# Kernel optimization log

Hardware: AMD Instinct MI355X
Metric: run time of the kernel (lower is better)

## Reference

```python
import jax, jax.numpy as jnp
import numpy as np

B, T, OB, AC, OBL, ACL, W = 2048, 128, 64, 8, 32, 16, 64
DT = 0.05   # spacing of save times
K = 2       # fixed Dopri5 substeps per interval (step size = ode_dt0 = 0.025)


def _mlp2(x, W0, b0, W1, b1):
    # eqx.nn.MLP with depth=1: in -> width (relu) -> out (identity)
    return jax.nn.relu(x @ W0.T + b0) @ W1.T + b1


def setup_inputs() -> dict:
    key = jax.random.key(0)
    ks = jax.random.split(key, 10)
    def lin(k, o, i, scale=1.0):
        return (jax.random.normal(k, (o, i), jnp.float32) * (scale / np.sqrt(i))).astype(jnp.float32)
    return {
        "encW0": lin(ks[0], W, OB), "encb0": jnp.zeros((W,), jnp.float32),
        "encW1": lin(ks[1], OBL, W), "encb1": jnp.zeros((OBL,), jnp.float32),
        "acW0": lin(ks[2], W, AC), "acb0": jnp.zeros((W,), jnp.float32),
        "acW1": lin(ks[3], ACL, W), "acb1": jnp.zeros((ACL,), jnp.float32),
        "dynW0": lin(ks[4], W, OBL + ACL), "dynb0": jnp.zeros((W,), jnp.float32),
        "dynW1": lin(ks[5], OBL, W, 0.5), "dynb1": jnp.zeros((OBL,), jnp.float32),
        "decW0": lin(ks[6], W, OBL), "decb0": jnp.zeros((W,), jnp.float32),
        "decW1": lin(ks[7], OB, W), "decb1": jnp.zeros((OB,), jnp.float32),
        "ob": jax.random.normal(ks[8], (B, OB), jnp.float32),
        "acs": jax.random.normal(ks[9], (B, T, AC), jnp.float32),
        "times": jnp.tile(jnp.arange(T, dtype=jnp.float32) * DT, (B, 1)),
    }


def _dopri5_step(f, t, y, h):
    k1 = f(t, y)
    k2 = f(t + h * (1. / 5.), y + h * ((1. / 5.) * k1))
    k3 = f(t + h * (3. / 10.), y + h * ((3. / 40.) * k1 + (9. / 40.) * k2))
    k4 = f(t + h * (4. / 5.), y + h * ((44. / 45.) * k1 - (56. / 15.) * k2 + (32. / 9.) * k3))
    k5 = f(t + h * (8. / 9.), y + h * ((19372. / 6561.) * k1 - (25360. / 2187.) * k2
                                       + (64448. / 6561.) * k3 - (212. / 729.) * k4))
    k6 = f(t + h, y + h * ((9017. / 3168.) * k1 - (355. / 33.) * k2 + (46732. / 5247.) * k3
                           + (49. / 176.) * k4 - (5103. / 18656.) * k5))
    return y + h * ((35. / 384.) * k1 + (500. / 1113.) * k3 + (125. / 192.) * k4
                    - (2187. / 6784.) * k5 + (11. / 84.) * k6)


def reference(encW0, encb0, encW1, encb1, acW0, acb0, acW1, acb1,
              dynW0, dynb0, dynW1, dynb1, decW0, decb0, decW1, decb1,
              ob, acs, times):
    ac_latents = _mlp2(acs, acW0, acb0, acW1, acb1)   # (B, T, ACL)
    y0 = _mlp2(ob, encW0, encb0, encW1, encb1)        # (B, OBL)

    def single(y0_i, acl_i, t_i):
        n = t_i.shape[0]

        def f(t, y):
            # piecewise-constant action latent: index of save-interval containing t
            idx = jnp.clip(jnp.searchsorted(t_i, t, side='right') - 1, 0, n - 1)
            return _mlp2(jnp.concatenate([y, acl_i[idx]]), dynW0, dynb0, dynW1, dynb1)

        def interval(y, tt):
            t0, t1 = tt
            h = (t1 - t0) / K
            def sub(yc, j):
                return _dopri5_step(f, t0 + j * h, yc, h), None
            y, _ = jax.lax.scan(sub, y, jnp.arange(K, dtype=t_i.dtype))
            return y, y

        _, ys = jax.lax.scan(interval, y0_i, (t_i[:-1], t_i[1:]))
        return jnp.concatenate([y0_i[None], ys], axis=0)   # (T, OBL)

    ys = jax.vmap(single)(y0, ac_latents, times)            # (B, T, OBL)
    return _mlp2(ys, decW0, decb0, decW1, decb1)            # (B, T, OB)
```

## Files before the change

kernel.cpp:

```cpp
#include <hip/hip_runtime.h>

#define NB 2048
#define NT 128

typedef float v2f __attribute__((ext_vector_type(2)));

static __device__ __forceinline__ v2f pkfma(v2f a, v2f b, v2f c) {
#if __has_builtin(__builtin_elementwise_fma)
    return __builtin_elementwise_fma(a, b, c);
#else
    v2f r; r.x = fmaf(a.x, b.x, c.x); r.y = fmaf(a.y, b.y, c.y); return r;
#endif
}
static __device__ __forceinline__ v2f mkv2(float x, float y) { v2f r; r.x = x; r.y = y; return r; }

__global__ __launch_bounds__(256, 4) void acl_kernel(
    const float* __restrict__ acs, const float* __restrict__ acW0,
    const float* __restrict__ acb0, const float* __restrict__ acW1,
    const float* __restrict__ acb1, float* __restrict__ aclout)
{
    __shared__ float sW0[64 * 8];
    __shared__ float sW1[16 * 64];
    __shared__ float sB0[64];
    __shared__ float sB1[16];
    const int tid = threadIdx.x;
    for (int i = tid; i < 64 * 8; i += 256) sW0[i] = acW0[i];
    for (int i = tid; i < 16 * 64; i += 256) sW1[i] = acW1[i];
    if (tid < 64) sB0[tid] = acb0[tid];
    if (tid < 16) sB1[tid] = acb1[tid];
    __syncthreads();

    const int row = blockIdx.x * 256 + tid;
    const float4 x0 = *(const float4*)&acs[row * 8];
    const float4 x1 = *(const float4*)&acs[row * 8 + 4];

    float o[16];
    #pragma unroll
    for (int m = 0; m < 16; ++m) o[m] = sB1[m];

    #pragma unroll
    for (int jc = 0; jc < 16; ++jc) {
        float hq[4];
        #pragma unroll
        for (int u = 0; u < 4; ++u) {
            const int j = jc * 4 + u;
            const float4 wa = *(const float4*)&sW0[j * 8];
            const float4 wb = *(const float4*)&sW0[j * 8 + 4];
            float hv = sB0[j];
            hv = fmaf(x0.x, wa.x, hv); hv = fmaf(x0.y, wa.y, hv);
            hv = fmaf(x0.z, wa.z, hv); hv = fmaf(x0.w, wa.w, hv);
            hv = fmaf(x1.x, wb.x, hv); hv = fmaf(x1.y, wb.y, hv);
            hv = fmaf(x1.z, wb.z, hv); hv = fmaf(x1.w, wb.w, hv);
            hq[u] = fmaxf(hv, 0.f);
        }
        #pragma unroll
        for (int m = 0; m < 16; ++m) {
            const float4 wv = *(const float4*)&sW1[m * 64 + jc * 4];
            o[m] = fmaf(hq[0], wv.x, o[m]);
            o[m] = fmaf(hq[1], wv.y, o[m]);
            o[m] = fmaf(hq[2], wv.z, o[m]);
            o[m] = fmaf(hq[3], wv.w, o[m]);
        }
    }
    float4* op = (float4*)&aclout[row * 16];
    op[0] = make_float4(o[0],  o[1],  o[2],  o[3]);
    op[1] = make_float4(o[4],  o[5],  o[6],  o[7]);
    op[2] = make_float4(o[8],  o[9],  o[10], o[11]);
    op[3] = make_float4(o[12], o[13], o[14], o[15]);
}

__global__ __launch_bounds__(256, 2) void ode_kernel(
    const float* __restrict__ encW0, const float* __restrict__ encb0,
    const float* __restrict__ encW1, const float* __restrict__ encb1,
    const float* __restrict__ dynW0, const float* __restrict__ dynb0,
    const float* __restrict__ dynW1, const float* __restrict__ dynb1,
    const float* __restrict__ ob,    const float* __restrict__ times,
    const float* __restrict__ aclws, float* __restrict__ yio)
{
    __shared__ float sEncW0T[64 * 64];
    __shared__ float sEncW1T[64 * 32];
    __shared__ float sW0s[64 * 32];
    __shared__ float sW1T[64 * 32];
    __shared__ float sM[64 * 64];
    __shared__ float sEncB0[64], sEncB1[32], sB1d[32];
    __shared__ float xbuf[4][64];
    __shared__ float hbuf[4][64];
    __shared__ float tbuf[4][NT];

    const int tid = threadIdx.x;
    for (int i = tid; i < 64 * 64; i += 256) { int r = i >> 6, c = i & 63; sEncW0T[c * 64 + r] = encW0[i]; }
    for (int i = tid; i < 32 * 64; i += 256) { int r = i >> 6, c = i & 63; sEncW1T[c * 32 + r] = encW1[i]; }
    for (int i = tid; i < 64 * 32; i += 256) { int j = i >> 5, mm = i & 31; sW0s[i] = dynW0[j * 48 + mm]; }
    for (int i = tid; i < 64 * 32; i += 256) { int c = i >> 5, mm = i & 31; sW1T[i] = dynW1[mm * 64 + c]; }
    if (tid < 64) { sEncB0[tid] = encb0[tid]; }
    if (tid < 32) { sEncB1[tid] = encb1[tid]; sB1d[tid] = dynb1[tid]; }
    __syncthreads();

    {
        const int j  = tid >> 2;
        const int cg = (tid & 3) * 16;
        float4 wr[8];
        #pragma unroll
        for (int q = 0; q < 8; ++q) wr[q] = *(const float4*)&sW0s[j * 32 + q * 4];
        #pragma unroll 2
        for (int k = 0; k < 16; ++k) {
            const int c = cg + k;
            v2f s0 = mkv2(0.f, 0.f), s1 = mkv2(0.f, 0.f);
            #pragma unroll
            for (int q = 0; q < 8; ++q) {
                const float4 t4 = *(const float4*)&sW1T[c * 32 + q * 4];
                s0 = pkfma(mkv2(t4.x, t4.y), mkv2(wr[q].x, wr[q].y), s0);
                s1 = pkfma(mkv2(t4.z, t4.w), mkv2(wr[q].z, wr[q].w), s1);
            }
            sM[j * 64 + c] = (s0.x + s1.x) + (s0.y + s1.y);
        }
    }
    __syncthreads();

    const int w    = tid >> 6;
    const int lane = tid & 63;
    const int bu   = __builtin_amdgcn_readfirstlane(blockIdx.x * 4 + w);
    const int m    = lane & 31;
    const int H    = lane & 32;

    float* __restrict__ xb = xbuf[w];
    float* __restrict__ hb = hbuf[w];

    float Mf[64];
    #pragma unroll
    for (int q = 0; q < 16; ++q) *(float4*)&Mf[q * 4] = *(const float4*)&sM[lane * 64 + q * 4];
    const v2f* Mp = (const v2f*)Mf;

    float w1rf[32];
    #pragma unroll
    for (int q = 0; q < 8; ++q)  *(float4*)&w1rf[q * 4] = *(const float4*)&dynW1[m * 64 + H + q * 4];
    const v2f* w1r = (const v2f*)w1rf;

    float wa[16];
    #pragma unroll
    for (int q = 0; q < 4; ++q) *(float4*)&wa[q * 4] = *(const float4*)&dynW0[lane * 48 + 32 + q * 4];
    const float b0r = dynb0[lane];
    const float b1r = dynb1[m];

    float vj = 0.f;
    #pragma unroll
    for (int q = 0; q < 8; ++q) {
        const float4 wv = *(const float4*)&dynW0[lane * 48 + q * 4];
        vj = fmaf(wv.x, sB1d[q * 4 + 0], vj); vj = fmaf(wv.y, sB1d[q * 4 + 1], vj);
        vj = fmaf(wv.z, sB1d[q * 4 + 2], vj); vj = fmaf(wv.w, sB1d[q * 4 + 3], vj);
    }

    tbuf[w][lane]      = times[bu * NT + lane];
    tbuf[w][64 + lane] = times[bu * NT + 64 + lane];
    __builtin_amdgcn_wave_barrier();

    auto gproj = [&](float hsv) -> float {
        __builtin_amdgcn_wave_barrier();
        hb[lane] = hsv;
        __builtin_amdgcn_wave_barrier();
        v2f A0 = mkv2(0.f, 0.f), A1 = mkv2(0.f, 0.f);
        v2f A2 = mkv2(0.f, 0.f), A3 = mkv2(0.f, 0.f);
        #pragma unroll
        for (int c = 0; c < 2; ++c) {
            float hr[32];
            #pragma unroll
            for (int q = 0; q < 8; ++q) *(float4*)&hr[q * 4] = *(const float4*)&hb[c * 32 + q * 4];
            const v2f* hp = (const v2f*)hr;
            const v2f* mp = Mp + c * 16;
            #pragma unroll
            for (int q = 0; q < 16; q += 4) {
                A0 = pkfma(hp[q],     mp[q],     A0);
                A1 = pkfma(hp[q + 1], mp[q + 1], A1);
                A2 = pkfma(hp[q + 2], mp[q + 2], A2);
                A3 = pkfma(hp[q + 3], mp[q + 3], A3);
            }
        }
        const v2f S = (A0 + A1) + (A2 + A3);
        return S.x + S.y + vj;
    };

    float y;
    {
        xb[lane] = ob[bu * 64 + lane];
        __builtin_amdgcn_wave_barrier();
        float4 xv[16];
        #pragma unroll
        for (int q = 0; q < 16; ++q) xv[q] = *(const float4*)&xb[q * 4];
        float a0 = sEncB0[lane], a1 = 0.f, a2 = 0.f, a3 = 0.f;
        #pragma unroll
        for (int q = 0; q < 16; ++q) {
            a0 = fmaf(xv[q].x, sEncW0T[(q * 4 + 0) * 64 + lane], a0);
            a1 = fmaf(xv[q].y, sEncW0T[(q * 4 + 1) * 64 + lane], a1);
            a2 = fmaf(xv[q].z, sEncW0T[(q * 4 + 2) * 64 + lane], a2);
            a3 = fmaf(xv[q].w, sEncW0T[(q * 4 + 3) * 64 + lane], a3);
        }
        const float hj = fmaxf((a0 + a1) + (a2 + a3), 0.f);
        hb[lane] = hj;
        __builtin_amdgcn_wave_barrier();
        float4 hv[8];
        #pragma unroll
        for (int q = 0; q < 8; ++q) hv[q] = *(const float4*)&hb[H + q * 4];
        float c0 = 0.f, c1 = 0.f, c2 = 0.f, c3 = 0.f;
        #pragma unroll
        for (int q = 0; q < 8; ++q) {
            c0 = fmaf(hv[q].x, sEncW1T[(H + q * 4 + 0) * 32 + m], c0);
            c1 = fmaf(hv[q].y, sEncW1T[(H + q * 4 + 1) * 32 + m], c1);
            c2 = fmaf(hv[q].z, sEncW1T[(H + q * 4 + 2) * 32 + m], c2);
            c3 = fmaf(hv[q].w, sEncW1T[(H + q * 4 + 3) * 32 + m], c3);
        }
        float part = (c0 + c1) + (c2 + c3);
        part += __shfl_xor(part, 32, 64);
        y = part + sEncB1[m];
    }

    float ystar = 0.f;
    {
        __builtin_amdgcn_wave_barrier();
        xb[m] = y;
        __builtin_amdgcn_wave_barrier();
        #pragma unroll
        for (int q = 0; q < 8; ++q) {
            const float4 wv = *(const float4*)&dynW0[lane * 48 + q * 4];
            const float4 xv = *(const float4*)&xb[q * 4];
            ystar = fmaf(wv.x, xv.x, ystar); ystar = fmaf(wv.y, xv.y, ystar);
            ystar = fmaf(wv.z, xv.z, ystar); ystar = fmaf(wv.w, xv.w, ystar);
        }
    }

    auto acl_part = [&](const float* __restrict__ ap) -> float {
        float ar[16];
        #pragma unroll
        for (int q = 0; q < 4; ++q) *(float4*)&ar[q * 4] = *(const float4*)&ap[q * 4];
        const v2f* a2 = (const v2f*)ar;
        const v2f* wq = (const v2f*)wa;
        v2f s0 = mkv2(0.f, 0.f), s1 = mkv2(0.f, 0.f);
        #pragma unroll
        for (int q = 0; q < 8; q += 2) {
            s0 = pkfma(a2[q],     wq[q],     s0);
            s1 = pkfma(a2[q + 1], wq[q + 1], s1);
        }
        const v2f s = s0 + s1;
        return s.x + s.y;
    };

    auto store_y = [&](float yv, int t) {
        if (lane < 32) yio[(size_t)(bu * NT + t) * 64 + lane] = yv;
    };

    float aclPartC = acl_part(aclws + (size_t)(bu * NT) * 16);
    store_y(y, 0);

    for (int i = 0; i < NT - 1; ++i) {
        const float t0v = tbuf[w][i];
        const float t1v = tbuf[w][i + 1];
        const float hh  = (t1v - t0v) * 0.5f;
        const float aclPartN = acl_part(aclws + (size_t)(bu * NT + i + 1) * 16);
        float haccS = 0.f;

        #pragma unroll 1
        for (int sub = 0; sub < 2; ++sub) {
            const float tsub  = t0v + (float)sub * hh;
            const bool  swap6 = (tsub + hh >= t1v);

            const float a1v = ystar + b0r + aclPartC;

            const float h1 = fmaxf(a1v, 0.f);
            const float g1 = hh * gproj(h1);
            const float h2 = fmaxf(fmaf(0.2f, g1, a1v), 0.f);
            const float g2 = hh * gproj(h2);
            const float h3 = fmaxf(fmaf(0.075f, g1, fmaf(0.225f, g2, a1v)), 0.f);
            const float g3 = hh * gproj(h3);
            const float h4 = fmaxf(
                fmaf((float)(44.0/45.0), g1,
                fmaf((float)(-56.0/15.0), g2,
                fmaf((float)(32.0/9.0), g3, a1v))), 0.f);
            const float g4 = hh * gproj(h4);
            const float h5 = fmaxf(
                fmaf((float)(19372.0/6561.0), g1,
                fmaf((float)(-25360.0/2187.0), g2,
                fmaf((float)(64448.0/6561.0), g3,
                fmaf((float)(-212.0/729.0), g4, a1v)))), 0.f);
            const float g5 = hh * gproj(h5);
            float a6v =
                fmaf((float)(9017.0/3168.0), g1,
                fmaf((float)(-355.0/33.0), g2,
                fmaf((float)(46732.0/5247.0), g3,
                fmaf((float)(49.0/176.0), g4,
                fmaf((float)(-5103.0/18656.0), g5, a1v)))));
            a6v += swap6 ? (aclPartN - aclPartC) : 0.f;
            const float h6 = fmaxf(a6v, 0.f);

            float ha = (float)(35.0/384.0) * h1;
            ha = fmaf((float)(500.0/1113.0),   h3, ha);
            ha = fmaf((float)(125.0/192.0),    h4, ha);
            ha = fmaf((float)(-2187.0/6784.0), h5, ha);
            ha = fmaf((float)(11.0/84.0),      h6, ha);

            const float gacc = gproj(ha);
            ystar = fmaf(hh, gacc, ystar);
            haccS += ha;
        }

        {
            __builtin_amdgcn_wave_barrier();
            hb[lane] = haccS;
            __builtin_amdgcn_wave_barrier();
            float hr[32];
            #pragma unroll
            for (int q = 0; q < 8; ++q) *(float4*)&hr[q * 4] = *(const float4*)&hb[H + q * 4];
            const v2f* hp = (const v2f*)hr;
            v2f c0 = mkv2(0.f, 0.f), c1 = mkv2(0.f, 0.f);
            #pragma unroll
            for (int q = 0; q < 16; q += 2) {
                c0 = pkfma(hp[q],     w1r[q],     c0);
                c1 = pkfma(hp[q + 1], w1r[q + 1], c1);
            }
            float part = (c0.x + c1.x) + (c0.y + c1.y);
            part += __shfl_xor(part, 32, 64);
            y = fmaf(hh, part + 2.f * b1r, y);
        }
        aclPartC = aclPartN;
        store_y(y, i + 1);
    }
}

__global__ __launch_bounds__(256, 2) void dec_kernel(
    const float* __restrict__ decW0, const float* __restrict__ decb0,
    const float* __restrict__ decW1, const float* __restrict__ decb1,
    float* __restrict__ yio)
{
    __shared__ float sW0[64 * 32];
    __shared__ float sW1T[64 * 64];
    __shared__ float sB0[64];
    __shared__ float sB1[64];
    const int tid = threadIdx.x;
    for (int i = tid; i < 64 * 32; i += 256) sW0[i] = decW0[i];
    for (int i = tid; i < 64 * 64; i += 256) { int n = i >> 6, j = i & 63; sW1T[j * 64 + n] = decW1[i]; }
    if (tid < 64) { sB0[tid] = decb0[tid]; sB1[tid] = decb1[tid]; }
    __syncthreads();

    const size_t row = (size_t)blockIdx.x * 256 + tid;
    float* rp = &yio[row * 64];

    float xr[32];
    #pragma unroll
    for (int q = 0; q < 8; ++q) *(float4*)&xr[q * 4] = *(const float4*)&rp[q * 4];

    v2f o2[32];
    #pragma unroll
    for (int n = 0; n < 32; ++n) o2[n] = mkv2(sB1[2 * n], sB1[2 * n + 1]);

    #pragma unroll 4
    for (int j = 0; j < 64; ++j) {
        v2f a0 = mkv2(sB0[j], 0.f), a1 = mkv2(0.f, 0.f);
        #pragma unroll
        for (int q = 0; q < 8; ++q) {
            const float4 wv = *(const float4*)&sW0[j * 32 + q * 4];
            a0 = pkfma(*(const v2f*)&xr[q * 4],     mkv2(wv.x, wv.y), a0);
            a1 = pkfma(*(const v2f*)&xr[q * 4 + 2], mkv2(wv.z, wv.w), a1);
        }
        const float hj = fmaxf((a0.x + a1.x) + (a0.y + a1.y), 0.f);
        const v2f h2 = mkv2(hj, hj);
        #pragma unroll
        for (int q = 0; q < 16; ++q) {
            const float4 wv = *(const float4*)&sW1T[j * 64 + q * 4];
            o2[2 * q]     = pkfma(h2, mkv2(wv.x, wv.y), o2[2 * q]);
            o2[2 * q + 1] = pkfma(h2, mkv2(wv.z, wv.w), o2[2 * q + 1]);
        }
    }

    #pragma unroll
    for (int q = 0; q < 16; ++q)
        *(float4*)&rp[q * 4] = make_float4(o2[2 * q].x, o2[2 * q].y,
                                           o2[2 * q + 1].x, o2[2 * q + 1].y);
}

extern "C" void kernel_launch(void* const* d_in, const int* in_sizes, int n_in,
                              void* d_out, int out_size, void* d_ws, size_t ws_size,
                              hipStream_t stream)
{
    const float* encW0 = (const float*)d_in[0];
    const float* encb0 = (const float*)d_in[1];
    const float* encW1 = (const float*)d_in[2];
    const float* encb1 = (const float*)d_in[3];
    const float* acW0  = (const float*)d_in[4];
    const float* acb0  = (const float*)d_in[5];
    const float* acW1  = (const float*)d_in[6];
    const float* acb1  = (const float*)d_in[7];
    const float* dynW0 = (const float*)d_in[8];
    const float* dynb0 = (const float*)d_in[9];
    const float* dynW1 = (const float*)d_in[10];
    const float* dynb1 = (const float*)d_in[11];
    const float* decW0 = (const float*)d_in[12];
    const float* decb0 = (const float*)d_in[13];
    const float* decW1 = (const float*)d_in[14];
    const float* decb1 = (const float*)d_in[15];
    const float* ob    = (const float*)d_in[16];
    const float* acs   = (const float*)d_in[17];
    const float* times = (const float*)d_in[18];
    float* out = (float*)d_out;
    float* acl = (float*)d_ws;

    acl_kernel<<<(NB * NT) / 256, 256, 0, stream>>>(acs, acW0, acb0, acW1, acb1, acl);
    ode_kernel<<<NB / 4, 256, 0, stream>>>(encW0, encb0, encW1, encb1,
                                           dynW0, dynb0, dynW1, dynb1,
                                           ob, times, acl, out);
    dec_kernel<<<(NB * NT) / 256, 256, 0, stream>>>(decW0, decb0, decW1, decb1, out);
}
```

Measured before the change: 689.5 us.

## Process two batch elements per wavefront in ODE kernel to reuse register weights

Each wavefront now integrates two independent trajectories together, interleaving their RK stages so every projection matvec reuses the register-resident M and W1 weights for both. The intent is to amortise weight register loads and expose independent instruction-level parallelism that hides the LDS and sequential-dependency latency of the stage chain. Grid is halved to NB/8 blocks and launch bounds drop to one block per CU minimum, which raises register pressure and reduces the number of wavefronts available for latency hiding. With 256 blocks on a 256-CU part, each CU gets only a single block.

```diff
diff --git a/kernel.cpp b/kernel.cpp
--- a/kernel.cpp
+++ b/kernel.cpp
@@ -69,7 +69,7 @@
     op[3] = make_float4(o[12], o[13], o[14], o[15]);
 }
 
-__global__ __launch_bounds__(256, 2) void ode_kernel(
+__global__ __launch_bounds__(256, 1) void ode_kernel(
     const float* __restrict__ encW0, const float* __restrict__ encb0,
     const float* __restrict__ encW1, const float* __restrict__ encb1,
     const float* __restrict__ dynW0, const float* __restrict__ dynb0,
@@ -83,15 +83,16 @@
     __shared__ float sW1T[64 * 32];
     __shared__ float sM[64 * 64];
     __shared__ float sEncB0[64], sEncB1[32], sB1d[32];
-    __shared__ float xbuf[4][64];
-    __shared__ float hbuf[4][64];
-    __shared__ float tbuf[4][NT];
+    __shared__ float xbuf[8][64];
+    __shared__ float hbuf[8][64];
+    __shared__ float tbuf[8 * NT];
 
     const int tid = threadIdx.x;
     for (int i = tid; i < 64 * 64; i += 256) { int r = i >> 6, c = i & 63; sEncW0T[c * 64 + r] = encW0[i]; }
     for (int i = tid; i < 32 * 64; i += 256) { int r = i >> 6, c = i & 63; sEncW1T[c * 32 + r] = encW1[i]; }
     for (int i = tid; i < 64 * 32; i += 256) { int j = i >> 5, mm = i & 31; sW0s[i] = dynW0[j * 48 + mm]; }
     for (int i = tid; i < 64 * 32; i += 256) { int c = i >> 5, mm = i & 31; sW1T[i] = dynW1[mm * 64 + c]; }
+    for (int i = tid; i < 8 * NT; i += 256) tbuf[i] = times[(size_t)blockIdx.x * 8 * NT + i];
     if (tid < 64) { sEncB0[tid] = encb0[tid]; }
     if (tid < 32) { sEncB1[tid] = encb1[tid]; sB1d[tid] = dynb1[tid]; }
     __syncthreads();
@@ -119,12 +120,16 @@
 
     const int w    = tid >> 6;
     const int lane = tid & 63;
-    const int bu   = __builtin_amdgcn_readfirstlane(blockIdx.x * 4 + w);
+    const int e0   = w * 2;
+    const int bu0  = __builtin_amdgcn_readfirstlane(blockIdx.x * 8 + e0);
+    const int bu1  = bu0 + 1;
     const int m    = lane & 31;
     const int H    = lane & 32;
 
-    float* __restrict__ xb = xbuf[w];
-    float* __restrict__ hb = hbuf[w];
+    float* __restrict__ xbA = xbuf[e0];
+    float* __restrict__ xbB = xbuf[e0 + 1];
+    float* __restrict__ hbA = hbuf[e0];
+    float* __restrict__ hbB = hbuf[e0 + 1];
 
     float Mf[64];
     #pragma unroll
@@ -150,37 +155,39 @@
         vj = fmaf(wv.z, sB1d[q * 4 + 2], vj); vj = fmaf(wv.w, sB1d[q * 4 + 3], vj);
     }
 
-    tbuf[w][lane]      = times[bu * NT + lane];
-    tbuf[w][64 + lane] = times[bu * NT + 64 + lane];
-    __builtin_amdgcn_wave_barrier();
-
-    auto gproj = [&](float hsv) -> float {
-        __builtin_amdgcn_wave_barrier();
-        hb[lane] = hsv;
+    auto gproj2 = [&](float hA, float hB, float& gA, float& gB) {
+        __builtin_amdgcn_wave_barrier();
+        hbA[lane] = hA;
+        hbB[lane] = hB;
         __builtin_amdgcn_wave_barrier();
         v2f A0 = mkv2(0.f, 0.f), A1 = mkv2(0.f, 0.f);
-        v2f A2 = mkv2(0.f, 0.f), A3 = mkv2(0.f, 0.f);
-        #pragma unroll
-        for (int c = 0; c < 2; ++c) {
-            float hr[32];
-            #pragma unroll
-            for (int q = 0; q < 8; ++q) *(float4*)&hr[q * 4] = *(const float4*)&hb[c * 32 + q * 4];
-            const v2f* hp = (const v2f*)hr;
-            const v2f* mp = Mp + c * 16;
-            #pragma unroll
-            for (int q = 0; q < 16; q += 4) {
-                A0 = pkfma(hp[q],     mp[q],     A0);
-                A1 = pkfma(hp[q + 1], mp[q + 1], A1);
-                A2 = pkfma(hp[q + 2], mp[q + 2], A2);
-                A3 = pkfma(hp[q + 3], mp[q + 3], A3);
+        v2f B0 = mkv2(0.f, 0.f), B1 = mkv2(0.f, 0.f);
+        #pragma unroll
+        for (int c = 0; c < 4; ++c) {
+            float hrA[16], hrB[16];
+            #pragma unroll
+            for (int q = 0; q < 4; ++q) *(float4*)&hrA[q * 4] = *(const float4*)&hbA[c * 16 + q * 4];
+            #pragma unroll
+            for (int q = 0; q < 4; ++q) *(float4*)&hrB[q * 4] = *(const float4*)&hbB[c * 16 + q * 4];
+            const v2f* hpA = (const v2f*)hrA;
+            const v2f* hpB = (const v2f*)hrB;
+            const v2f* mp  = Mp + c * 8;
+            #pragma unroll
+            for (int q = 0; q < 8; q += 2) {
+                A0 = pkfma(hpA[q],     mp[q],     A0);
+                A1 = pkfma(hpA[q + 1], mp[q + 1], A1);
+                B0 = pkfma(hpB[q],     mp[q],     B0);
+                B1 = pkfma(hpB[q + 1], mp[q + 1], B1);
             }
         }
-        const v2f S = (A0 + A1) + (A2 + A3);
-        return S.x + S.y + vj;
+        const v2f SA = A0 + A1;
+        const v2f SB = B0 + B1;
+        gA = SA.x + SA.y + vj;
+        gB = SB.x + SB.y + vj;
     };
 
-    float y;
-    {
+    auto encode = [&](int bu, float* xb, float* hb) -> float {
+        __builtin_amdgcn_wave_barrier();
         xb[lane] = ob[bu * 64 + lane];
         __builtin_amdgcn_wave_barrier();
         float4 xv[16];
@@ -195,6 +202,7 @@
             a3 = fmaf(xv[q].w, sEncW0T[(q * 4 + 3) * 64 + lane], a3);
         }
         const float hj = fmaxf((a0 + a1) + (a2 + a3), 0.f);
+        __builtin_amdgcn_wave_barrier();
         hb[lane] = hj;
         __builtin_amdgcn_wave_barrier();
         float4 hv[8];
@@ -210,22 +218,28 @@
         }
         float part = (c0 + c1) + (c2 + c3);
         part += __shfl_xor(part, 32, 64);
-        y = part + sEncB1[m];
-    }
-
-    float ystar = 0.f;
-    {
-        __builtin_amdgcn_wave_barrier();
-        xb[m] = y;
-        __builtin_amdgcn_wave_barrier();
+        return part + sEncB1[m];
+    };
+
+    auto ystar_init = [&](float yv, float* xb) -> float {
+        __builtin_amdgcn_wave_barrier();
+        xb[m] = yv;
+        __builtin_amdgcn_wave_barrier();
+        float ys = 0.f;
         #pragma unroll
         for (int q = 0; q < 8; ++q) {
             const float4 wv = *(const float4*)&dynW0[lane * 48 + q * 4];
             const float4 xv = *(const float4*)&xb[q * 4];
-            ystar = fmaf(wv.x, xv.x, ystar); ystar = fmaf(wv.y, xv.y, ystar);
-            ystar = fmaf(wv.z, xv.z, ystar); ystar = fmaf(wv.w, xv.w, ystar);
-        }
-    }
+            ys = fmaf(wv.x, xv.x, ys); ys = fmaf(wv.y, xv.y, ys);
+            ys = fmaf(wv.z, xv.z, ys); ys = fmaf(wv.w, xv.w, ys);
+        }
+        return ys;
+    };
+
+    float yA = encode(bu0, xbA, hbA);
+    float yB = encode(bu1, xbB, hbB);
+    float ystarA = ystar_init(yA, xbA);
+    float ystarB = ystar_init(yB, xbB);
 
     auto acl_part = [&](const float* __restrict__ ap) -> float {
         float ar[16];
@@ -243,84 +257,141 @@
         return s.x + s.y;
     };
 
-    auto store_y = [&](float yv, int t) {
+    auto store_y = [&](float yv, int bu, int t) {
         if (lane < 32) yio[(size_t)(bu * NT + t) * 64 + lane] = yv;
     };
 
-    float aclPartC = acl_part(aclws + (size_t)(bu * NT) * 16);
-    store_y(y, 0);
+    float aclCA = acl_part(aclws + (size_t)(bu0 * NT) * 16);
+    float aclCB = acl_part(aclws + (size_t)(bu1 * NT) * 16);
+    store_y(yA, bu0, 0);
+    store_y(yB, bu1, 0);
+
+    const int tb0 = e0 * NT;
+    const int tb1 = (e0 + 1) * NT;
 
     for (int i = 0; i < NT - 1; ++i) {
-        const float t0v = tbuf[w][i];
-        const float t1v = tbuf[w][i + 1];
-        const float hh  = (t1v - t0v) * 0.5f;
-        const float aclPartN = acl_part(aclws + (size_t)(bu * NT + i + 1) * 16);
-        float haccS = 0.f;
+        const float t0A = tbuf[tb0 + i], t1A = tbuf[tb0 + i + 1];
+        const float t0B = tbuf[tb1 + i], t1B = tbuf[tb1 + i + 1];
+        const float hhA = (t1A - t0A) * 0.5f;
+        const float hhB = (t1B - t0B) * 0.5f;
+        const float aclNA = acl_part(aclws + (size_t)(bu0 * NT + i + 1) * 16);
+        const float aclNB = acl_part(aclws + (size_t)(bu1 * NT + i + 1) * 16);
+        float haccSA = 0.f, haccSB = 0.f;
 
         #pragma unroll 1
         for (int sub = 0; sub < 2; ++sub) {
-            const float tsub  = t0v + (float)sub * hh;
-            const bool  swap6 = (tsub + hh >= t1v);
-
-            const float a1v = ystar + b0r + aclPartC;
-
-            const float h1 = fmaxf(a1v, 0.f);
-            const float g1 = hh * gproj(h1);
-            const float h2 = fmaxf(fmaf(0.2f, g1, a1v), 0.f);
-            const float g2 = hh * gproj(h2);
-            const float h3 = fmaxf(fmaf(0.075f, g1, fmaf(0.225f, g2, a1v)), 0.f);
-            const float g3 = hh * gproj(h3);
-            const float h4 = fmaxf(
-                fmaf((float)(44.0/45.0), g1,
-                fmaf((float)(-56.0/15.0), g2,
-                fmaf((float)(32.0/9.0), g3, a1v))), 0.f);
-            const float g4 = hh * gproj(h4);
-            const float h5 = fmaxf(
-                fmaf((float)(19372.0/6561.0), g1,
-                fmaf((float)(-25360.0/2187.0), g2,
-                fmaf((float)(64448.0/6561.0), g3,
-                fmaf((float)(-212.0/729.0), g4, a1v)))), 0.f);
-            const float g5 = hh * gproj(h5);
-            float a6v =
-                fmaf((float)(9017.0/3168.0), g1,
-                fmaf((float)(-355.0/33.0), g2,
-                fmaf((float)(46732.0/5247.0), g3,
-                fmaf((float)(49.0/176.0), g4,
-                fmaf((float)(-5103.0/18656.0), g5, a1v)))));
-            a6v += swap6 ? (aclPartN - aclPartC) : 0.f;
-            const float h6 = fmaxf(a6v, 0.f);
-
-            float ha = (float)(35.0/384.0) * h1;
-            ha = fmaf((float)(500.0/1113.0),   h3, ha);
-            ha = fmaf((float)(125.0/192.0),    h4, ha);
-            ha = fmaf((float)(-2187.0/6784.0), h5, ha);
-            ha = fmaf((float)(11.0/84.0),      h6, ha);
-
-            const float gacc = gproj(ha);
-            ystar = fmaf(hh, gacc, ystar);
-            haccS += ha;
+            const float tsubA = t0A + (float)sub * hhA;
+            const float tsubB = t0B + (float)sub * hhB;
+            const bool swap6A = (tsubA + hhA >= t1A);
+            const bool swap6B = (tsubB + hhB >= t1B);
+
+            const float a1A = ystarA + b0r + aclCA;
+            const float a1B = ystarB + b0r + aclCB;
+
+            float g1A, g1B, g2A, g2B, g3A, g3B, g4A, g4B, g5A, g5B;
+
+            const float h1A = fmaxf(a1A, 0.f);
+            const float h1B = fmaxf(a1B, 0.f);
+            gproj2(h1A, h1B, g1A, g1B); g1A *= hhA; g1B *= hhB;
+
+            const float h2A = fmaxf(fmaf(0.2f, g1A, a1A), 0.f);
+            const float h2B = fmaxf(fmaf(0.2f, g1B, a1B), 0.f);
+            gproj2(h2A, h2B, g2A, g2B); g2A *= hhA; g2B *= hhB;
+
+            const float h3A = fmaxf(fmaf(0.075f, g1A, fmaf(0.225f, g2A, a1A)), 0.f);
+            const float h3B = fmaxf(fmaf(0.075f, g1B, fmaf(0.225f, g2B, a1B)), 0.f);
+            gproj2(h3A, h3B, g3A, g3B); g3A *= hhA; g3B *= hhB;
+
+            const float h4A = fmaxf(
+                fmaf((float)(44.0/45.0), g1A,
+                fmaf((float)(-56.0/15.0), g2A,
+                fmaf((float)(32.0/9.0), g3A, a1A))), 0.f);
+            const float h4B = fmaxf(
+                fmaf((float)(44.0/45.0), g1B,
+                fmaf((float)(-56.0/15.0), g2B,
+                fmaf((float)(32.0/9.0), g3B, a1B))), 0.f);
+            gproj2(h4A, h4B, g4A, g4B); g4A *= hhA; g4B *= hhB;
+
+            const float h5A = fmaxf(
+                fmaf((float)(19372.0/6561.0), g1A,
+                fmaf((float)(-25360.0/2187.0), g2A,
+                fmaf((float)(64448.0/6561.0), g3A,
+                fmaf((float)(-212.0/729.0), g4A, a1A)))), 0.f);
+            const float h5B = fmaxf(
+                fmaf((float)(19372.0/6561.0), g1B,
+                fmaf((float)(-25360.0/2187.0), g2B,
+                fmaf((float)(64448.0/6561.0), g3B,
+                fmaf((float)(-212.0/729.0), g4B, a1B)))), 0.f);
+            gproj2(h5A, h5B, g5A, g5B); g5A *= hhA; g5B *= hhB;
+
+            float a6A =
+                fmaf((float)(9017.0/3168.0), g1A,
+                fmaf((float)(-355.0/33.0), g2A,
+                fmaf((float)(46732.0/5247.0), g3A,
+                fmaf((float)(49.0/176.0), g4A,
+                fmaf((float)(-5103.0/18656.0), g5A, a1A)))));
+            float a6B =
+                fmaf((float)(9017.0/3168.0), g1B,
+                fmaf((float)(-355.0/33.0), g2B,
+                fmaf((float)(46732.0/5247.0), g3B,
+                fmaf((float)(49.0/176.0), g4B,
+                fmaf((float)(-5103.0/18656.0), g5B, a1B)))));
+            a6A += swap6A ? (aclNA - aclCA) : 0.f;
+            a6B += swap6B ? (aclNB - aclCB) : 0.f;
+            const float h6A = fmaxf(a6A, 0.f);
+            const float h6B = fmaxf(a6B, 0.f);
+
+            float haA = (float)(35.0/384.0) * h1A;
+            haA = fmaf((float)(500.0/1113.0),   h3A, haA);
+            haA = fmaf((float)(125.0/192.0),    h4A, haA);
+            haA = fmaf((float)(-2187.0/6784.0), h5A, haA);
+            haA = fmaf((float)(11.0/84.0),      h6A, haA);
+            float haB = (float)(35.0/384.0) * h1B;
+            haB = fmaf((float)(500.0/1113.0),   h3B, haB);
+            haB = fmaf((float)(125.0/192.0),    h4B, haB);
+            haB = fmaf((float)(-2187.0/6784.0), h5B, haB);
+            haB = fmaf((float)(11.0/84.0),      h6B, haB);
+
+            float gaA, gaB;
+            gproj2(haA, haB, gaA, gaB);
+            ystarA = fmaf(hhA, gaA, ystarA);
+            ystarB = fmaf(hhB, gaB, ystarB);
+            haccSA += haA;
+            haccSB += haB;
         }
 
         {
             __builtin_amdgcn_wave_barrier();
-            hb[lane] = haccS;
+            hbA[lane] = haccSA;
+            hbB[lane] = haccSB;
             __builtin_amdgcn_wave_barrier();
-            float hr[32];
-            #pragma unroll
-            for (int q = 0; q < 8; ++q) *(float4*)&hr[q * 4] = *(const float4*)&hb[H + q * 4];
-            const v2f* hp = (const v2f*)hr;
-            v2f c0 = mkv2(0.f, 0.f), c1 = mkv2(0.f, 0.f);
+            float hrA[32], hrB[32];
+            #pragma unroll
+            for (int q = 0; q < 8; ++q) *(float4*)&hrA[q * 4] = *(const float4*)&hbA[H + q * 4];
+            #pragma unroll
+            for (int q = 0; q < 8; ++q) *(float4*)&hrB[q * 4] = *(const float4*)&hbB[H + q * 4];
+            const v2f* hpA = (const v2f*)hrA;
+            const v2f* hpB = (const v2f*)hrB;
+            v2f cA0 = mkv2(0.f, 0.f), cA1 = mkv2(0.f, 0.f);
+            v2f cB0 = mkv2(0.f, 0.f), cB1 = mkv2(0.f, 0.f);
             #pragma unroll
             for (int q = 0; q < 16; q += 2) {
-                c0 = pkfma(hp[q],     w1r[q],     c0);
-                c1 = pkfma(hp[q + 1], w1r[q + 1], c1);
+                cA0 = pkfma(hpA[q],     w1r[q],     cA0);
+                cA1 = pkfma(hpA[q + 1], w1r[q + 1], cA1);
+                cB0 = pkfma(hpB[q],     w1r[q],     cB0);
+                cB1 = pkfma(hpB[q + 1], w1r[q + 1], cB1);
             }
-            float part = (c0.x + c1.x) + (c0.y + c1.y);
-            part += __shfl_xor(part, 32, 64);
-            y = fmaf(hh, part + 2.f * b1r, y);
-        }
-        aclPartC = aclPartN;
-        store_y(y, i + 1);
+            float partA = (cA0.x + cA1.x) + (cA0.y + cA1.y);
+            float partB = (cB0.x + cB1.x) + (cB0.y + cB1.y);
+            partA += __shfl_xor(partA, 32, 64);
+            partB += __shfl_xor(partB, 32, 64);
+            yA = fmaf(hhA, partA + 2.f * b1r, yA);
+            yB = fmaf(hhB, partB + 2.f * b1r, yB);
+        }
+        aclCA = aclNA;
+        aclCB = aclNB;
+        store_y(yA, bu0, i + 1);
+        store_y(yB, bu1, i + 1);
     }
 }
 
@@ -402,7 +473,7 @@
     float* acl = (float*)d_ws;
 
     acl_kernel<<<(NB * NT) / 256, 256, 0, stream>>>(acs, acW0, acb0, acW1, acb1, acl);
-    ode_kernel<<<NB / 4, 256, 0, stream>>>(encW0, encb0, encW1, encb1,
+    ode_kernel<<<NB / 8, 256, 0, stream>>>(encW0, encb0, encW1, encb1,
                                            dynW0, dynb0, dynW1, dynb1,
                                            ob, times, acl, out);
     dec_kernel<<<(NB * NT) / 256, 256, 0, stream>>>(decW0, decb0, decW1, decb1, out);
```

Result: slower. 865.1 us (+25.5%).
